# Kernel optimization log

Measured on AMD Instinct MI355X. Metric: run time of the kernel, lower is better.

Reference implementation:

```python
import jax, jax.numpy as jnp
import numpy as np

B, L, D = 8, 4096, 512  # batch, seq_len (power of 2), in_features
R_MIN, R_MAX = 0.9, 0.999


def setup_inputs() -> dict:
    key = jax.random.key(0)
    k1, k2, k3 = jax.random.split(key, 3)
    inputs = jax.random.normal(k1, (B, L, D), dtype=jnp.float32)
    # Linear layers: i_dense D->2D, o_dense 2D->D (torch Linear: y = x @ W.T + b)
    Wi = jax.random.normal(k2, (2 * D, D), dtype=jnp.float32) / np.sqrt(D)
    bi = jnp.zeros((2 * D,), dtype=jnp.float32)
    Wo = jax.random.normal(k3, (D, 2 * D), dtype=jnp.float32) / np.sqrt(2 * D)
    bo = jnp.zeros((D,), dtype=jnp.float32)
    # LRU param init, exactly as in the torch module
    rng = np.random.RandomState(0)
    u1 = rng.random_sample(D)
    u2 = rng.random_sample(D)
    v_log = np.log(-0.5 * np.log(u1 * (R_MAX ** 2 - R_MIN ** 2) + R_MIN ** 2))
    theta_log = np.log(u2 * np.pi * 2)
    gamma_log = np.log(np.sqrt(1 - np.exp(-np.exp(v_log)) ** 2))
    params_log = jnp.asarray(np.stack([v_log, theta_log, gamma_log]), dtype=jnp.float32)
    return {"inputs": inputs, "Wi": Wi, "bi": bi, "Wo": Wo, "bo": bo,
            "params_log": params_log}


def reference(inputs, Wi, bi, Wo, bo, params_log):
    b, lin, d = inputs.shape
    u = inputs @ Wi.T + bi                       # [B, L, 2D]
    params = jnp.exp(params_log)                 # [3, D]
    v, theta, gamma = params[0], params[1], params[2]
    log2_L = int(np.ceil(np.log2(lin)))
    Lp = 2 ** log2_L
    # interleaved (real, imag) pairs -> complex state
    u = u.reshape(b, lin, d, 2)
    x = jax.lax.complex(u[..., 0], u[..., 1])    # [B, L, D] complex64
    if Lp > lin:
        x = jnp.pad(x, ((0, 0), (0, Lp - lin), (0, 0)))
    # Blelloch-style doubling scan: after stage i, each block of length 2^i
    # holds the prefix-scanned values x_t = lam*x_{t-1} + u_t within the block.
    for i in range(1, log2_L + 1):
        l = 2 ** i
        xr = x.reshape(b * Lp // l, l, d)
        x1, x2 = xr[:, : l // 2], xr[:, l // 2 :]
        pos = jnp.arange(1, l // 2 + 1, dtype=jnp.float32)        # [l/2]
        lambs = jnp.exp(jax.lax.complex(-pos[:, None] * v,
                                        pos[:, None] * theta))   # [l/2, D]
        x2 = x2 + lambs * x1[:, -1:]
        x = jnp.concatenate([x1, x2], axis=1).reshape(b, Lp, d)
    x = x[:, :lin] * gamma.astype(jnp.complex64)
    xr = jnp.concatenate([jnp.real(x), jnp.imag(x)], axis=-1)     # [B, L, 2D]
    out = xr @ Wo.T + bo
    return jax.nn.relu(out)
```

## Files before the change

kernel.cpp:

```cpp
#include <hip/hip_runtime.h>
#include <cstdint>
#include <cstddef>

typedef unsigned short u16;
typedef unsigned int   u32;

typedef short bf16x8 __attribute__((ext_vector_type(8)));
typedef float f32x4  __attribute__((ext_vector_type(4)));

__device__ __forceinline__ u16 f2bf(float f) {
  u32 u = __float_as_uint(f);
  u += 0x7fffu + ((u >> 16) & 1u);
  return (u16)(u >> 16);
}
__device__ __forceinline__ float bflo(u32 w) { return __uint_as_float((w & 0xffffu) << 16); }
__device__ __forceinline__ float bfhi(u32 w) { return __uint_as_float(w & 0xffff0000u); }

#define GLB_AS(p) ((const __attribute__((address_space(1))) void*)(p))
#define LDS_AS(p) ((__attribute__((address_space(3))) void*)(p))

__global__ __launch_bounds__(256)
void conv3_f32_bf16(const float* __restrict__ in, u16* __restrict__ a,
                    const float* __restrict__ wi, u16* __restrict__ wib,
                    const float* __restrict__ wo, u16* __restrict__ wob)
{
  long i = (long)blockIdx.x * 256 + threadIdx.x;
  const float* src; u16* dst;
  if (i < 4194304L) { src = in; dst = a; }
  else if (i < 4325376L) { i -= 4194304L; src = wi; dst = wib; }
  else { i -= 4325376L; if (i >= 131072L) return; src = wo; dst = wob; }
  float4 v = ((const float4*)src)[i];
  u32 lo = (u32)f2bf(v.x) | ((u32)f2bf(v.y) << 16);
  u32 hi = (u32)f2bf(v.z) | ((u32)f2bf(v.w) << 16);
  ((uint2*)dst)[i] = make_uint2(lo, hi);
}

template<int N, int K, int LOGNB, int OUT_BF16, int RELU>
__global__ __launch_bounds__(512, 4)
void gemm_w2(const u16* __restrict__ A, const u16* __restrict__ Bw,
             const float* __restrict__ bias, void* __restrict__ Cout)
{
  __shared__ __align__(16) u16 As[3][256 * 32];
  __shared__ __align__(16) u16 Bs[3][128 * 32];

  const int tid  = threadIdx.x;
  const int lane = tid & 63;
  const int wave = tid >> 6;
  const int bid  = blockIdx.x;
  const int xcd  = bid & 7;
  const int s    = bid >> 3;
  const int m0 = (xcd * 16 + (s >> LOGNB)) * 256;
  const int n0 = (s & ((1 << LOGNB) - 1)) * 128;
  const int wm = (wave & 3) * 64;
  const int wn = (wave >> 2) * 64;

  f32x4 acc[4][4];
#pragma unroll
  for (int i = 0; i < 4; ++i)
#pragma unroll
    for (int j = 0; j < 4; ++j) acc[i][j] = f32x4{0.f, 0.f, 0.f, 0.f};

  const u16* Ap[2]; const u16* Bp; int ldsA[2]; int ldsB;
#pragma unroll
  for (int i = 0; i < 2; ++i) {
    int g = i * 512 + tid;
    int r = g >> 2;
    int koff = ((g & 3) ^ ((r >> 1) & 3)) << 3;
    Ap[i]   = A + (size_t)(m0 + r) * K + koff;
    ldsA[i] = (i * 512 + wave * 64) * 8;
  }
  {
    int g = tid;
    int r = g >> 2;
    int koff = ((g & 3) ^ ((r >> 1) & 3)) << 3;
    Bp   = Bw + (size_t)(n0 + r) * K + koff;
    ldsB = (wave * 64) * 8;
  }

  const int fm = lane & 15;
  const int q  = lane >> 4;
  int aoff[4], boff[4];
#pragma unroll
  for (int i = 0; i < 4; ++i) {
    int m = wm + i * 16 + fm;
    aoff[i] = (m * 4 + (q ^ ((m >> 1) & 3))) * 8;
    int n = wn + i * 16 + fm;
    boff[i] = (n * 4 + (q ^ ((n >> 1) & 3))) * 8;
  }

  auto stage = [&](int buf, int kt) {
    __builtin_amdgcn_global_load_lds(GLB_AS(Ap[0] + kt), LDS_AS(&As[buf][ldsA[0]]), 16, 0, 0);
    __builtin_amdgcn_global_load_lds(GLB_AS(Ap[1] + kt), LDS_AS(&As[buf][ldsA[1]]), 16, 0, 0);
    __builtin_amdgcn_global_load_lds(GLB_AS(Bp    + kt), LDS_AS(&Bs[buf][ldsB]),    16, 0, 0);
  };
  auto compute = [&](int buf) {
    bf16x8 af[4], bfr[4];
#pragma unroll
    for (int i = 0; i < 4; ++i) { af[i]  = *(const bf16x8*)&As[buf][aoff[i]];
                                  bfr[i] = *(const bf16x8*)&Bs[buf][boff[i]]; }
#pragma unroll
    for (int mi = 0; mi < 4; ++mi)
#pragma unroll
      for (int ni = 0; ni < 4; ++ni)
        acc[mi][ni] = __builtin_amdgcn_mfma_f32_16x16x32_bf16(af[mi], bfr[ni],
                                                              acc[mi][ni], 0, 0, 0);
  };

  constexpr int NT = K / 32;
  stage(0, 0);
  stage(1, 32);
#pragma unroll
  for (int t = 0; t < NT - 1; ++t) {
    asm volatile("s_waitcnt vmcnt(3)" ::: "memory");
    __builtin_amdgcn_s_barrier();
    if (t + 2 < NT) stage((t + 2) % 3, (t + 2) * 32);
    compute(t % 3);
  }
  asm volatile("s_waitcnt vmcnt(0)" ::: "memory");
  __builtin_amdgcn_s_barrier();
  compute((NT - 1) % 3);

  const int colL = lane & 15;
  const int rowQ = (lane >> 4) * 4;
#pragma unroll
  for (int mi = 0; mi < 4; ++mi) {
#pragma unroll
    for (int ni = 0; ni < 4; ++ni) {
      int col  = n0 + wn + ni * 16 + colL;
      int rowb = m0 + wm + mi * 16 + rowQ;
      float bv = bias[col];
#pragma unroll
      for (int r = 0; r < 4; ++r) {
        float v = acc[mi][ni][r] + bv;
        if (RELU) v = fmaxf(v, 0.f);
        size_t idx = (size_t)(rowb + r) * N + col;
        if (OUT_BF16) ((u16*)Cout)[idx] = f2bf(v);
        else          ((float*)Cout)[idx] = v;
      }
    }
  }
}

__global__ __launch_bounds__(256)
void scan_chunk_end(const u16* __restrict__ u, const float* __restrict__ plog,
                    float2* __restrict__ e)
{
  const int t = threadIdx.x;
  const int c = blockIdx.x;
  const int b = blockIdx.y;
  float2 vl = ((const float2*)plog)[t];
  float2 tl = ((const float2*)plog)[256 + t];
  float v0 = expf(vl.x), v1 = expf(vl.y);
  float t0 = expf(tl.x), t1 = expf(tl.y);
  float m0 = expf(-v0), m1 = expf(-v1);
  float lr0 = m0 * cosf(t0), li0 = m0 * sinf(t0);
  float lr1 = m1 * cosf(t1), li1 = m1 * sinf(t1);
  const uint2* up = (const uint2*)u;
  size_t idx = (size_t)(b * 4096 + c * 32) * 256 + t;
  float h0r = 0.f, h0i = 0.f, h1r = 0.f, h1i = 0.f;
#pragma unroll 8
  for (int s = 0; s < 32; ++s) {
    uint2 w = up[idx]; idx += 256;
    float u0r = bflo(w.x), u0i = bfhi(w.x);
    float u1r = bflo(w.y), u1i = bfhi(w.y);
    float n0r = fmaf(lr0, h0r, fmaf(-li0, h0i, u0r));
    float n0i = fmaf(lr0, h0i, fmaf( li0, h0r, u0i));
    float n1r = fmaf(lr1, h1r, fmaf(-li1, h1i, u1r));
    float n1i = fmaf(lr1, h1i, fmaf( li1, h1r, u1i));
    h0r = n0r; h0i = n0i; h1r = n1r; h1i = n1i;
  }
  ((float4*)e)[(size_t)(b * 128 + c) * 256 + t] = make_float4(h0r, h0i, h1r, h1i);
}

__global__ __launch_bounds__(256)
void scan_mid(const float* __restrict__ plog, float4* __restrict__ e)
{
  const int t = threadIdx.x;
  const int b = blockIdx.x;
  float2 vl = ((const float2*)plog)[t];
  float2 tl = ((const float2*)plog)[256 + t];
  float v0 = expf(vl.x), v1 = expf(vl.y);
  float t0 = expf(tl.x), t1 = expf(tl.y);
  float Lm0 = expf(-32.f * v0), Lm1 = expf(-32.f * v1);
  float La0 = 32.f * t0,        La1 = 32.f * t1;
  float Lr0 = Lm0 * cosf(La0), Li0 = Lm0 * sinf(La0);
  float Lr1 = Lm1 * cosf(La1), Li1 = Lm1 * sinf(La1);
  float h0r = 0.f, h0i = 0.f, h1r = 0.f, h1i = 0.f;
  size_t base = (size_t)(b * 128) * 256 + t;
#pragma unroll 4
  for (int c = 0; c < 128; ++c) {
    float4 ec = e[base + (size_t)c * 256];
    float n0r = fmaf(Lr0, h0r, fmaf(-Li0, h0i, ec.x));
    float n0i = fmaf(Lr0, h0i, fmaf( Li0, h0r, ec.y));
    float n1r = fmaf(Lr1, h1r, fmaf(-Li1, h1i, ec.z));
    float n1i = fmaf(Lr1, h1i, fmaf( Li1, h1r, ec.w));
    h0r = n0r; h0i = n0i; h1r = n1r; h1i = n1i;
    e[base + (size_t)c * 256] = make_float4(h0r, h0i, h1r, h1i);
  }
}

__global__ __launch_bounds__(256)
void scan_out2(const u16* __restrict__ u, const float* __restrict__ plog,
               const float4* __restrict__ e, u16* __restrict__ xr)
{
  const int t = threadIdx.x;
  const int c = blockIdx.x;
  const int b = blockIdx.y;
  float2 vl = ((const float2*)plog)[t];
  float2 tl = ((const float2*)plog)[256 + t];
  float2 gl = ((const float2*)plog)[512 + t];
  float v0 = expf(vl.x), v1 = expf(vl.y);
  float t0 = expf(tl.x), t1 = expf(tl.y);
  float g0 = expf(gl.x), g1 = expf(gl.y);
  float m0 = expf(-v0), m1 = expf(-v1);
  float lr0 = m0 * cosf(t0), li0 = m0 * sinf(t0);
  float lr1 = m1 * cosf(t1), li1 = m1 * sinf(t1);

  float h0r = 0.f, h0i = 0.f, h1r = 0.f, h1i = 0.f;
  if (c > 0) {
    float4 ec = e[(size_t)(b * 128 + c - 1) * 256 + t];
    h0r = ec.x; h0i = ec.y; h1r = ec.z; h1i = ec.w;
  }

  const uint2* up = (const uint2*)u;
  u32* xp = (u32*)xr;
  size_t uidx = (size_t)(b * 4096 + c * 32) * 256 + t;
  size_t xidx = (size_t)(b * 4096 + c * 32) * 512 + t;
#pragma unroll 8
  for (int s = 0; s < 32; ++s) {
    uint2 w = up[uidx]; uidx += 256;
    float u0r = bflo(w.x), u0i = bfhi(w.x);
    float u1r = bflo(w.y), u1i = bfhi(w.y);
    float n0r = fmaf(lr0, h0r, fmaf(-li0, h0i, u0r));
    float n0i = fmaf(lr0, h0i, fmaf( li0, h0r, u0i));
    float n1r = fmaf(lr1, h1r, fmaf(-li1, h1i, u1r));
    float n1i = fmaf(lr1, h1i, fmaf( li1, h1r, u1i));
    h0r = n0r; h0i = n0i; h1r = n1r; h1i = n1i;
    xp[xidx]       = (u32)f2bf(g0 * h0r) | ((u32)f2bf(g1 * h1r) << 16);
    xp[xidx + 256] = (u32)f2bf(g0 * h0i) | ((u32)f2bf(g1 * h1i) << 16);
    xidx += 512;
  }
}

extern "C" void kernel_launch(void* const* d_in, const int* in_sizes, int n_in,
                              void* d_out, int out_size, void* d_ws, size_t ws_size,
                              hipStream_t stream)
{
  (void)in_sizes; (void)n_in; (void)out_size; (void)ws_size;
  const float* inputs = (const float*)d_in[0];
  const float* Wi     = (const float*)d_in[1];
  const float* bi     = (const float*)d_in[2];
  const float* Wo     = (const float*)d_in[3];
  const float* bo     = (const float*)d_in[4];
  const float* plog   = (const float*)d_in[5];

  char* ws = (char*)d_ws;
  u16*    xrA   = (u16*)(ws);
  u16*    u_bf  = (u16*)(ws + 67108864ull);
  u16*    Wi_bf = (u16*)(ws + 134217728ull);
  u16*    Wo_bf = (u16*)(ws + 135266304ull);
  float2* e_b   = (float2*)(ws + 136314880ull);

  conv3_f32_bf16<<<17408, 256, 0, stream>>>(inputs, xrA, Wi, Wi_bf, Wo, Wo_bf);

  gemm_w2<1024, 512, 3, 1, 0><<<1024, 512, 0, stream>>>(xrA, Wi_bf, bi, u_bf);

  scan_chunk_end<<<dim3(128, 8), 256, 0, stream>>>(u_bf, plog, e_b);
  scan_mid<<<8, 256, 0, stream>>>(plog, (float4*)e_b);
  scan_out2<<<dim3(128, 8), 256, 0, stream>>>(u_bf, plog, (const float4*)e_b, xrA);

  gemm_w2<512, 1024, 2, 0, 1><<<512, 512, 0, stream>>>(xrA, Wo_bf, bo, d_out);
}
```

Before: 252.5 us.

## Fuse three-pass chunked scan into one kernel with flag-based decoupled lookback

Replaces the chunk-end, mid and output scan kernels with one kernel. Each block keeps its 32 timesteps of u in registers, publishes its local chunk-end state with a release flag, then spins on the flags of earlier chunks and combines their states using powers of lambda^32, processing four chunks at a time. This removes two launches, the serial scan_mid pass and the second read of u, at the cost of spin-waiting that relies on earlier blocks being scheduled first, a flags memset, and O(c) lookback work per block. The conversion kernel also becomes a grid-stride loop with fewer blocks.

After: 767.5 us. 204% more time.

```diff
diff --git a/kernel.cpp b/kernel.cpp
--- a/kernel.cpp
+++ b/kernel.cpp
@@ -24,15 +24,18 @@
                     const float* __restrict__ wi, u16* __restrict__ wib,
                     const float* __restrict__ wo, u16* __restrict__ wob)
 {
-  long i = (long)blockIdx.x * 256 + threadIdx.x;
-  const float* src; u16* dst;
-  if (i < 4194304L) { src = in; dst = a; }
-  else if (i < 4325376L) { i -= 4194304L; src = wi; dst = wib; }
-  else { i -= 4325376L; if (i >= 131072L) return; src = wo; dst = wob; }
-  float4 v = ((const float4*)src)[i];
-  u32 lo = (u32)f2bf(v.x) | ((u32)f2bf(v.y) << 16);
-  u32 hi = (u32)f2bf(v.z) | ((u32)f2bf(v.w) << 16);
-  ((uint2*)dst)[i] = make_uint2(lo, hi);
+  const long total = 4456448L;
+  for (long i = (long)blockIdx.x * 256 + threadIdx.x; i < total;
+       i += (long)gridDim.x * 256) {
+    long j = i; const float* src; u16* dst;
+    if (j < 4194304L) { src = in; dst = a; }
+    else if (j < 4325376L) { j -= 4194304L; src = wi; dst = wib; }
+    else { j -= 4325376L; src = wo; dst = wob; }
+    float4 v = ((const float4*)src)[j];
+    u32 lo = (u32)f2bf(v.x) | ((u32)f2bf(v.y) << 16);
+    u32 hi = (u32)f2bf(v.z) | ((u32)f2bf(v.w) << 16);
+    ((uint2*)dst)[j] = make_uint2(lo, hi);
+  }
 }
 
 template<int N, int K, int LOGNB, int OUT_BF16, int RELU>
@@ -142,70 +145,14 @@
 }
 
 __global__ __launch_bounds__(256)
-void scan_chunk_end(const u16* __restrict__ u, const float* __restrict__ plog,
-                    float2* __restrict__ e)
+void scan_fused(const u16* __restrict__ u, const float* __restrict__ plog,
+                float4* __restrict__ e, u32* __restrict__ flags,
+                u16* __restrict__ xr)
 {
   const int t = threadIdx.x;
   const int c = blockIdx.x;
   const int b = blockIdx.y;
-  float2 vl = ((const float2*)plog)[t];
-  float2 tl = ((const float2*)plog)[256 + t];
-  float v0 = expf(vl.x), v1 = expf(vl.y);
-  float t0 = expf(tl.x), t1 = expf(tl.y);
-  float m0 = expf(-v0), m1 = expf(-v1);
-  float lr0 = m0 * cosf(t0), li0 = m0 * sinf(t0);
-  float lr1 = m1 * cosf(t1), li1 = m1 * sinf(t1);
-  const uint2* up = (const uint2*)u;
-  size_t idx = (size_t)(b * 4096 + c * 32) * 256 + t;
-  float h0r = 0.f, h0i = 0.f, h1r = 0.f, h1i = 0.f;
-#pragma unroll 8
-  for (int s = 0; s < 32; ++s) {
-    uint2 w = up[idx]; idx += 256;
-    float u0r = bflo(w.x), u0i = bfhi(w.x);
-    float u1r = bflo(w.y), u1i = bfhi(w.y);
-    float n0r = fmaf(lr0, h0r, fmaf(-li0, h0i, u0r));
-    float n0i = fmaf(lr0, h0i, fmaf( li0, h0r, u0i));
-    float n1r = fmaf(lr1, h1r, fmaf(-li1, h1i, u1r));
-    float n1i = fmaf(lr1, h1i, fmaf( li1, h1r, u1i));
-    h0r = n0r; h0i = n0i; h1r = n1r; h1i = n1i;
-  }
-  ((float4*)e)[(size_t)(b * 128 + c) * 256 + t] = make_float4(h0r, h0i, h1r, h1i);
-}
-
-__global__ __launch_bounds__(256)
-void scan_mid(const float* __restrict__ plog, float4* __restrict__ e)
-{
-  const int t = threadIdx.x;
-  const int b = blockIdx.x;
-  float2 vl = ((const float2*)plog)[t];
-  float2 tl = ((const float2*)plog)[256 + t];
-  float v0 = expf(vl.x), v1 = expf(vl.y);
-  float t0 = expf(tl.x), t1 = expf(tl.y);
-  float Lm0 = expf(-32.f * v0), Lm1 = expf(-32.f * v1);
-  float La0 = 32.f * t0,        La1 = 32.f * t1;
-  float Lr0 = Lm0 * cosf(La0), Li0 = Lm0 * sinf(La0);
-  float Lr1 = Lm1 * cosf(La1), Li1 = Lm1 * sinf(La1);
-  float h0r = 0.f, h0i = 0.f, h1r = 0.f, h1i = 0.f;
-  size_t base = (size_t)(b * 128) * 256 + t;
-#pragma unroll 4
-  for (int c = 0; c < 128; ++c) {
-    float4 ec = e[base + (size_t)c * 256];
-    float n0r = fmaf(Lr0, h0r, fmaf(-Li0, h0i, ec.x));
-    float n0i = fmaf(Lr0, h0i, fmaf( Li0, h0r, ec.y));
-    float n1r = fmaf(Lr1, h1r, fmaf(-Li1, h1i, ec.z));
-    float n1i = fmaf(Lr1, h1i, fmaf( Li1, h1r, ec.w));
-    h0r = n0r; h0i = n0i; h1r = n1r; h1i = n1i;
-    e[base + (size_t)c * 256] = make_float4(h0r, h0i, h1r, h1i);
-  }
-}
-
-__global__ __launch_bounds__(256)
-void scan_out2(const u16* __restrict__ u, const float* __restrict__ plog,
-               const float4* __restrict__ e, u16* __restrict__ xr)
-{
-  const int t = threadIdx.x;
-  const int c = blockIdx.x;
-  const int b = blockIdx.y;
+
   float2 vl = ((const float2*)plog)[t];
   float2 tl = ((const float2*)plog)[256 + t];
   float2 gl = ((const float2*)plog)[512 + t];
@@ -216,21 +163,110 @@
   float lr0 = m0 * cosf(t0), li0 = m0 * sinf(t0);
   float lr1 = m1 * cosf(t1), li1 = m1 * sinf(t1);
 
+  const uint2* up = (const uint2*)u;
+  size_t uidx = (size_t)(b * 4096 + c * 32) * 256 + t;
+  uint2 ur[32];
+#pragma unroll
+  for (int s = 0; s < 32; ++s) { ur[s] = up[uidx]; uidx += 256; }
+
   float h0r = 0.f, h0i = 0.f, h1r = 0.f, h1i = 0.f;
+#pragma unroll
+  for (int s = 0; s < 32; ++s) {
+    float u0r = bflo(ur[s].x), u0i = bfhi(ur[s].x);
+    float u1r = bflo(ur[s].y), u1i = bfhi(ur[s].y);
+    float n0r = fmaf(lr0, h0r, fmaf(-li0, h0i, u0r));
+    float n0i = fmaf(lr0, h0i, fmaf( li0, h0r, u0i));
+    float n1r = fmaf(lr1, h1r, fmaf(-li1, h1i, u1r));
+    float n1i = fmaf(lr1, h1i, fmaf( li1, h1r, u1i));
+    h0r = n0r; h0i = n0i; h1r = n1r; h1i = n1i;
+  }
+
+  const int fbase = b * 128;
+  e[(size_t)(fbase + c) * 256 + t] = make_float4(h0r, h0i, h1r, h1i);
+  __syncthreads();
+  if (t == 0) {
+    __threadfence();
+    __hip_atomic_store(&flags[fbase + c], 1u, __ATOMIC_RELEASE,
+                       __HIP_MEMORY_SCOPE_AGENT);
+  }
+
+  float cr0 = 0.f, ci0 = 0.f, cr1 = 0.f, ci1 = 0.f;
   if (c > 0) {
-    float4 ec = e[(size_t)(b * 128 + c - 1) * 256 + t];
-    h0r = ec.x; h0i = ec.y; h1r = ec.z; h1i = ec.w;
-  }
-
-  const uint2* up = (const uint2*)u;
+    float Lm0 = expf(-32.f * v0), Lm1 = expf(-32.f * v1);
+    float La0 = 32.f * t0,        La1 = 32.f * t1;
+    float P1r0 = Lm0 * cosf(La0), P1i0 = Lm0 * sinf(La0);
+    float P1r1 = Lm1 * cosf(La1), P1i1 = Lm1 * sinf(La1);
+    float P2r0 = P1r0*P1r0 - P1i0*P1i0, P2i0 = 2.f*P1r0*P1i0;
+    float P2r1 = P1r1*P1r1 - P1i1*P1i1, P2i1 = 2.f*P1r1*P1i1;
+    float P3r0 = P2r0*P1r0 - P2i0*P1i0, P3i0 = P2r0*P1i0 + P2i0*P1r0;
+    float P3r1 = P2r1*P1r1 - P2i1*P1i1, P3i1 = P2r1*P1i1 + P2i1*P1r1;
+    float P4r0 = P2r0*P2r0 - P2i0*P2i0, P4i0 = 2.f*P2r0*P2i0;
+    float P4r1 = P2r1*P2r1 - P2i1*P2i1, P4i1 = 2.f*P2r1*P2i1;
+
+    float Wr0 = 1.f, Wi0 = 0.f, Wr1 = 1.f, Wi1 = 0.f;
+    int i = c - 1;
+    while (i >= 0 && (i & 3) != 3) {
+      if (t == 0)
+        while (__hip_atomic_load(&flags[fbase + i], __ATOMIC_ACQUIRE,
+                                 __HIP_MEMORY_SCOPE_AGENT) == 0u) {}
+      __syncthreads();
+      float4 ec = e[(size_t)(fbase + i) * 256 + t];
+      cr0 = fmaf(Wr0, ec.x, fmaf(-Wi0, ec.y, cr0));
+      ci0 = fmaf(Wr0, ec.y, fmaf( Wi0, ec.x, ci0));
+      cr1 = fmaf(Wr1, ec.z, fmaf(-Wi1, ec.w, cr1));
+      ci1 = fmaf(Wr1, ec.w, fmaf( Wi1, ec.z, ci1));
+      float nr0 = Wr0*P1r0 - Wi0*P1i0, ni0 = Wr0*P1i0 + Wi0*P1r0;
+      float nr1 = Wr1*P1r1 - Wi1*P1i1, ni1 = Wr1*P1i1 + Wi1*P1r1;
+      Wr0 = nr0; Wi0 = ni0; Wr1 = nr1; Wi1 = ni1;
+      --i;
+    }
+    while (i >= 3) {
+      int j = i - 3;
+      if (t == 0) {
+        for (;;) {
+          u32 f0 = __hip_atomic_load(&flags[fbase + j],     __ATOMIC_ACQUIRE, __HIP_MEMORY_SCOPE_AGENT);
+          u32 f1 = __hip_atomic_load(&flags[fbase + j + 1], __ATOMIC_ACQUIRE, __HIP_MEMORY_SCOPE_AGENT);
+          u32 f2 = __hip_atomic_load(&flags[fbase + j + 2], __ATOMIC_ACQUIRE, __HIP_MEMORY_SCOPE_AGENT);
+          u32 f3 = __hip_atomic_load(&flags[fbase + j + 3], __ATOMIC_ACQUIRE, __HIP_MEMORY_SCOPE_AGENT);
+          if (f0 & f1 & f2 & f3) break;
+        }
+      }
+      __syncthreads();
+      float4 e3 = e[(size_t)(fbase + i)     * 256 + t];
+      float4 e2 = e[(size_t)(fbase + i - 1) * 256 + t];
+      float4 e1 = e[(size_t)(fbase + i - 2) * 256 + t];
+      float4 e0 = e[(size_t)(fbase + i - 3) * 256 + t];
+      float a0r = e3.x, a0i = e3.y, a1r = e3.z, a1i = e3.w;
+      a0r = fmaf(P1r0, e2.x, fmaf(-P1i0, e2.y, a0r));
+      a0i = fmaf(P1r0, e2.y, fmaf( P1i0, e2.x, a0i));
+      a1r = fmaf(P1r1, e2.z, fmaf(-P1i1, e2.w, a1r));
+      a1i = fmaf(P1r1, e2.w, fmaf( P1i1, e2.z, a1i));
+      a0r = fmaf(P2r0, e1.x, fmaf(-P2i0, e1.y, a0r));
+      a0i = fmaf(P2r0, e1.y, fmaf( P2i0, e1.x, a0i));
+      a1r = fmaf(P2r1, e1.z, fmaf(-P2i1, e1.w, a1r));
+      a1i = fmaf(P2r1, e1.w, fmaf( P2i1, e1.z, a1i));
+      a0r = fmaf(P3r0, e0.x, fmaf(-P3i0, e0.y, a0r));
+      a0i = fmaf(P3r0, e0.y, fmaf( P3i0, e0.x, a0i));
+      a1r = fmaf(P3r1, e0.z, fmaf(-P3i1, e0.w, a1r));
+      a1i = fmaf(P3r1, e0.w, fmaf( P3i1, e0.z, a1i));
+      cr0 = fmaf(Wr0, a0r, fmaf(-Wi0, a0i, cr0));
+      ci0 = fmaf(Wr0, a0i, fmaf( Wi0, a0r, ci0));
+      cr1 = fmaf(Wr1, a1r, fmaf(-Wi1, a1i, cr1));
+      ci1 = fmaf(Wr1, a1i, fmaf( Wi1, a1r, ci1));
+      float nr0 = Wr0*P4r0 - Wi0*P4i0, ni0 = Wr0*P4i0 + Wi0*P4r0;
+      float nr1 = Wr1*P4r1 - Wi1*P4i1, ni1 = Wr1*P4i1 + Wi1*P4r1;
+      Wr0 = nr0; Wi0 = ni0; Wr1 = nr1; Wi1 = ni1;
+      i -= 4;
+    }
+  }
+
+  h0r = cr0; h0i = ci0; h1r = cr1; h1i = ci1;
   u32* xp = (u32*)xr;
-  size_t uidx = (size_t)(b * 4096 + c * 32) * 256 + t;
   size_t xidx = (size_t)(b * 4096 + c * 32) * 512 + t;
-#pragma unroll 8
+#pragma unroll
   for (int s = 0; s < 32; ++s) {
-    uint2 w = up[uidx]; uidx += 256;
-    float u0r = bflo(w.x), u0i = bfhi(w.x);
-    float u1r = bflo(w.y), u1i = bfhi(w.y);
+    float u0r = bflo(ur[s].x), u0i = bfhi(ur[s].x);
+    float u1r = bflo(ur[s].y), u1i = bfhi(ur[s].y);
     float n0r = fmaf(lr0, h0r, fmaf(-li0, h0i, u0r));
     float n0i = fmaf(lr0, h0i, fmaf( li0, h0r, u0i));
     float n1r = fmaf(lr1, h1r, fmaf(-li1, h1i, u1r));
@@ -259,15 +295,16 @@
   u16*    u_bf  = (u16*)(ws + 67108864ull);
   u16*    Wi_bf = (u16*)(ws + 134217728ull);
   u16*    Wo_bf = (u16*)(ws + 135266304ull);
-  float2* e_b   = (float2*)(ws + 136314880ull);
-
-  conv3_f32_bf16<<<17408, 256, 0, stream>>>(inputs, xrA, Wi, Wi_bf, Wo, Wo_bf);
+  float4* e_b   = (float4*)(ws + 136314880ull);
+  u32*    flags = (u32*)(ws + 140509184ull);
+
+  hipMemsetAsync(flags, 0, 8 * 128 * sizeof(u32), stream);
+
+  conv3_f32_bf16<<<4096, 256, 0, stream>>>(inputs, xrA, Wi, Wi_bf, Wo, Wo_bf);
 
   gemm_w2<1024, 512, 3, 1, 0><<<1024, 512, 0, stream>>>(xrA, Wi_bf, bi, u_bf);
 
-  scan_chunk_end<<<dim3(128, 8), 256, 0, stream>>>(u_bf, plog, e_b);
-  scan_mid<<<8, 256, 0, stream>>>(plog, (float4*)e_b);
-  scan_out2<<<dim3(128, 8), 256, 0, stream>>>(u_bf, plog, (const float4*)e_b, xrA);
+  scan_fused<<<dim3(128, 8), 256, 0, stream>>>(u_bf, plog, e_b, flags, xrA);
 
   gemm_w2<512, 1024, 2, 0, 1><<<512, 512, 0, stream>>>(xrA, Wo_bf, bo, d_out);
 }
```

## Rework GEMM to 256x256 tiles with BK=64 ping-pong quadrant schedule

Applied to the files above, without the earlier changes.

Replaces the 256x128 triple-buffered GEMM with a 256x256 tile, K-step of 64 and double buffering. Each wave now computes 128x64, and work is split into four MFMA quadrants interleaved with staged loads, barriers and setprio. The aim is better operand reuse per LDS byte and overlap of global loads with MFMA work. The cost is more registers (launch bounds lowered to 2 blocks per CU) and half as many blocks, which risks lower occupancy and worse tail balance, especially for the second GEMM with only 256 blocks.

New measurement: 274.4 us. +8.7%, slower.

```diff
diff --git a/kernel.cpp b/kernel.cpp
--- a/kernel.cpp
+++ b/kernel.cpp
@@ -36,12 +36,12 @@
 }
 
 template<int N, int K, int LOGNB, int OUT_BF16, int RELU>
-__global__ __launch_bounds__(512, 4)
-void gemm_w2(const u16* __restrict__ A, const u16* __restrict__ Bw,
+__global__ __launch_bounds__(512, 2)
+void gemm_8p(const u16* __restrict__ A, const u16* __restrict__ Bw,
              const float* __restrict__ bias, void* __restrict__ Cout)
 {
-  __shared__ __align__(16) u16 As[3][256 * 32];
-  __shared__ __align__(16) u16 Bs[3][128 * 32];
+  __shared__ __align__(16) u16 As[2][16384];
+  __shared__ __align__(16) u16 Bs[2][16384];
 
   const int tid  = threadIdx.x;
   const int lane = tid & 63;
@@ -50,88 +50,125 @@
   const int xcd  = bid & 7;
   const int s    = bid >> 3;
   const int m0 = (xcd * 16 + (s >> LOGNB)) * 256;
-  const int n0 = (s & ((1 << LOGNB) - 1)) * 128;
-  const int wm = (wave & 3) * 64;
-  const int wn = (wave >> 2) * 64;
-
-  f32x4 acc[4][4];
-#pragma unroll
-  for (int i = 0; i < 4; ++i)
+  const int n0 = (s & ((1 << LOGNB) - 1)) * 256;
+  const int wmr = (wave >> 2) * 128;
+  const int wn  = (wave & 3) * 64;
+
+  f32x4 acc[8][4];
+#pragma unroll
+  for (int i = 0; i < 8; ++i)
 #pragma unroll
     for (int j = 0; j < 4; ++j) acc[i][j] = f32x4{0.f, 0.f, 0.f, 0.f};
 
-  const u16* Ap[2]; const u16* Bp; int ldsA[2]; int ldsB;
-#pragma unroll
-  for (int i = 0; i < 2; ++i) {
-    int g = i * 512 + tid;
-    int r = g >> 2;
-    int koff = ((g & 3) ^ ((r >> 1) & 3)) << 3;
-    Ap[i]   = A + (size_t)(m0 + r) * K + koff;
-    ldsA[i] = (i * 512 + wave * 64) * 8;
-  }
-  {
-    int g = tid;
-    int r = g >> 2;
-    int koff = ((g & 3) ^ ((r >> 1) & 3)) << 3;
-    Bp   = Bw + (size_t)(n0 + r) * K + koff;
-    ldsB = (wave * 64) * 8;
-  }
+  const int koff = (((tid & 3) ^ ((tid >> 3) & 3)) << 3);
+  const u16* ApH[2]; const u16* BpH[2];
+#pragma unroll
+  for (int h = 0; h < 2; ++h) {
+    int r = 128 * h + (tid >> 2);
+    ApH[h] = A  + (size_t)(m0 + r) * K + koff;
+    BpH[h] = Bw + (size_t)(n0 + r) * K + koff;
+  }
+  const int ldsWave = wave * 64;
 
   const int fm = lane & 15;
   const int q  = lane >> 4;
-  int aoff[4], boff[4];
+  int aoffs[4][2], boffs[4][2];
 #pragma unroll
   for (int i = 0; i < 4; ++i) {
-    int m = wm + i * 16 + fm;
-    aoff[i] = (m * 4 + (q ^ ((m >> 1) & 3))) * 8;
-    int n = wn + i * 16 + fm;
-    boff[i] = (n * 4 + (q ^ ((n >> 1) & 3))) * 8;
-  }
-
-  auto stage = [&](int buf, int kt) {
-    __builtin_amdgcn_global_load_lds(GLB_AS(Ap[0] + kt), LDS_AS(&As[buf][ldsA[0]]), 16, 0, 0);
-    __builtin_amdgcn_global_load_lds(GLB_AS(Ap[1] + kt), LDS_AS(&As[buf][ldsA[1]]), 16, 0, 0);
-    __builtin_amdgcn_global_load_lds(GLB_AS(Bp    + kt), LDS_AS(&Bs[buf][ldsB]),    16, 0, 0);
-  };
-  auto compute = [&](int buf) {
-    bf16x8 af[4], bfr[4];
-#pragma unroll
-    for (int i = 0; i < 4; ++i) { af[i]  = *(const bf16x8*)&As[buf][aoff[i]];
-                                  bfr[i] = *(const bf16x8*)&Bs[buf][boff[i]]; }
-#pragma unroll
-    for (int mi = 0; mi < 4; ++mi)
-#pragma unroll
-      for (int ni = 0; ni < 4; ++ni)
-        acc[mi][ni] = __builtin_amdgcn_mfma_f32_16x16x32_bf16(af[mi], bfr[ni],
-                                                              acc[mi][ni], 0, 0, 0);
-  };
-
-  constexpr int NT = K / 32;
-  stage(0, 0);
-  stage(1, 32);
-#pragma unroll
-  for (int t = 0; t < NT - 1; ++t) {
-    asm volatile("s_waitcnt vmcnt(3)" ::: "memory");
-    __builtin_amdgcn_s_barrier();
-    if (t + 2 < NT) stage((t + 2) % 3, (t + 2) * 32);
-    compute(t % 3);
-  }
-  asm volatile("s_waitcnt vmcnt(0)" ::: "memory");
-  __builtin_amdgcn_s_barrier();
-  compute((NT - 1) % 3);
+    int m = wmr + i * 16 + fm;
+    int n = wn  + i * 16 + fm;
+#pragma unroll
+    for (int kk = 0; kk < 2; ++kk) {
+      aoffs[i][kk] = (kk * 1024 + m * 4 + (q ^ ((m >> 1) & 3))) * 8;
+      boffs[i][kk] = (kk * 1024 + n * 4 + (q ^ ((n >> 1) & 3))) * 8;
+    }
+  }
+
+  bf16x8 aH[4][2];
+  bf16x8 bF[4][2];
+
+  auto stageA = [&](int buf, int kt, int h) {
+#pragma unroll
+    for (int kk = 0; kk < 2; ++kk)
+      __builtin_amdgcn_global_load_lds(GLB_AS(ApH[h] + kt + kk * 32),
+          LDS_AS(&As[buf][(kk * 1024 + 512 * h + ldsWave) * 8]), 16, 0, 0);
+  };
+  auto stageB = [&](int buf, int kt, int h) {
+#pragma unroll
+    for (int kk = 0; kk < 2; ++kk)
+      __builtin_amdgcn_global_load_lds(GLB_AS(BpH[h] + kt + kk * 32),
+          LDS_AS(&Bs[buf][(kk * 1024 + 512 * h + ldsWave) * 8]), 16, 0, 0);
+  };
+  auto readA = [&](int buf, int mh) {
+#pragma unroll
+    for (int mf = 0; mf < 4; ++mf)
+#pragma unroll
+      for (int kk = 0; kk < 2; ++kk)
+        aH[mf][kk] = *(const bf16x8*)&As[buf][aoffs[mf][kk] + mh * 2048];
+  };
+  auto readB = [&](int buf, int nh) {
+#pragma unroll
+    for (int nf = 0; nf < 2; ++nf)
+#pragma unroll
+      for (int kk = 0; kk < 2; ++kk)
+        bF[nh * 2 + nf][kk] = *(const bf16x8*)&Bs[buf][boffs[nh * 2 + nf][kk]];
+  };
+  auto mfmaQ = [&](int mh, int nh) {
+#pragma unroll
+    for (int mf = 0; mf < 4; ++mf)
+#pragma unroll
+      for (int nf = 0; nf < 2; ++nf)
+#pragma unroll
+        for (int kk = 0; kk < 2; ++kk)
+          acc[mh * 4 + mf][nh * 2 + nf] =
+            __builtin_amdgcn_mfma_f32_16x16x32_bf16(aH[mf][kk], bF[nh * 2 + nf][kk],
+                                                    acc[mh * 4 + mf][nh * 2 + nf], 0, 0, 0);
+  };
+
+  constexpr int NT = K / 64;
+  stageA(0, 0, 0); stageA(0, 0, 1); stageB(0, 0, 0); stageB(0, 0, 1);
+  int cur = 0;
+  for (int t = 0; t < NT; ++t) {
+    const int nxt = cur ^ 1;
+    const bool pre = (t + 1 < NT);
+    const int ktn = (t + 1) * 64;
+    if (pre) { stageA(nxt, ktn, 0); stageB(nxt, ktn, 0); }
+    if (pre) asm volatile("s_waitcnt vmcnt(4)" ::: "memory");
+    else     asm volatile("s_waitcnt vmcnt(0)" ::: "memory");
+    __builtin_amdgcn_s_barrier();
+    readA(cur, 0); readB(cur, 0);
+    asm volatile("s_waitcnt lgkmcnt(0)" ::: "memory");
+    __builtin_amdgcn_sched_barrier(0);
+    __builtin_amdgcn_s_setprio(1); mfmaQ(0, 0); __builtin_amdgcn_s_setprio(0);
+    __builtin_amdgcn_s_barrier();
+    if (pre) { stageA(nxt, ktn, 1); stageB(nxt, ktn, 1); }
+    readB(cur, 1);
+    asm volatile("s_waitcnt lgkmcnt(0)" ::: "memory");
+    __builtin_amdgcn_sched_barrier(0);
+    __builtin_amdgcn_s_setprio(1); mfmaQ(0, 1); __builtin_amdgcn_s_setprio(0);
+    __builtin_amdgcn_s_barrier();
+    readA(cur, 1);
+    asm volatile("s_waitcnt lgkmcnt(0)" ::: "memory");
+    __builtin_amdgcn_sched_barrier(0);
+    __builtin_amdgcn_s_setprio(1); mfmaQ(1, 0); __builtin_amdgcn_s_setprio(0);
+    __builtin_amdgcn_s_barrier();
+    __builtin_amdgcn_s_setprio(1); mfmaQ(1, 1); __builtin_amdgcn_s_setprio(0);
+    __builtin_amdgcn_s_barrier();
+    cur = nxt;
+  }
 
   const int colL = lane & 15;
   const int rowQ = (lane >> 4) * 4;
 #pragma unroll
-  for (int mi = 0; mi < 4; ++mi) {
-#pragma unroll
-    for (int ni = 0; ni < 4; ++ni) {
-      int col  = n0 + wn + ni * 16 + colL;
-      int rowb = m0 + wm + mi * 16 + rowQ;
+  for (int mf = 0; mf < 8; ++mf) {
+#pragma unroll
+    for (int nf = 0; nf < 4; ++nf) {
+      int col  = n0 + wn + nf * 16 + colL;
+      int rowb = m0 + wmr + mf * 16 + rowQ;
       float bv = bias[col];
 #pragma unroll
       for (int r = 0; r < 4; ++r) {
-        float v = acc[mi][ni][r] + bv;
+        float v = acc[mf][nf][r] + bv;
         if (RELU) v = fmaxf(v, 0.f);
         size_t idx = (size_t)(rowb + r) * N + col;
         if (OUT_BF16) ((u16*)Cout)[idx] = f2bf(v);
@@ -263,11 +300,11 @@
 
   conv3_f32_bf16<<<17408, 256, 0, stream>>>(inputs, xrA, Wi, Wi_bf, Wo, Wo_bf);
 
-  gemm_w2<1024, 512, 3, 1, 0><<<1024, 512, 0, stream>>>(xrA, Wi_bf, bi, u_bf);
+  gemm_8p<1024, 512, 2, 1, 0><<<512, 512, 0, stream>>>(xrA, Wi_bf, bi, u_bf);
 
   scan_chunk_end<<<dim3(128, 8), 256, 0, stream>>>(u_bf, plog, e_b);
   scan_mid<<<8, 256, 0, stream>>>(plog, (float4*)e_b);
   scan_out2<<<dim3(128, 8), 256, 0, stream>>>(u_bf, plog, (const float4*)e_b, xrA);
 
-  gemm_w2<512, 1024, 2, 0, 1><<<512, 512, 0, stream>>>(xrA, Wo_bf, bo, d_out);
-}
+  gemm_8p<512, 1024, 1, 0, 1><<<256, 512, 0, stream>>>(xrA, Wo_bf, bo, d_out);
+}
```

## Fuse fp32-to-bf16 input conversion into the first GEMM's A-tile loading

Applied to the files above, without the earlier changes.

Drops the separate pass that converted the 64 MB fp32 activation tensor to bf16. The first GEMM now loads fp32 A tiles through registers, converts them to bf16 and writes them to LDS, while B still uses direct global-to-LDS loads. This removes a full read-write pass over the activations. In exchange the GEMM reads twice as many A bytes, uses register staging with a two-buffer pipeline instead of three, and per-element epilogue stores.

New measurement: 276.8 us. 1.1x slower.

```diff
diff --git a/kernel.cpp b/kernel.cpp
--- a/kernel.cpp
+++ b/kernel.cpp
@@ -20,19 +20,141 @@
 #define LDS_AS(p) ((__attribute__((address_space(3))) void*)(p))
 
 __global__ __launch_bounds__(256)
-void conv3_f32_bf16(const float* __restrict__ in, u16* __restrict__ a,
-                    const float* __restrict__ wi, u16* __restrict__ wib,
+void conv2_f32_bf16(const float* __restrict__ wi, u16* __restrict__ wib,
                     const float* __restrict__ wo, u16* __restrict__ wob)
 {
   long i = (long)blockIdx.x * 256 + threadIdx.x;
   const float* src; u16* dst;
-  if (i < 4194304L) { src = in; dst = a; }
-  else if (i < 4325376L) { i -= 4194304L; src = wi; dst = wib; }
-  else { i -= 4325376L; if (i >= 131072L) return; src = wo; dst = wob; }
+  if (i < 131072L) { src = wi; dst = wib; }
+  else { i -= 131072L; src = wo; dst = wob; }
   float4 v = ((const float4*)src)[i];
   u32 lo = (u32)f2bf(v.x) | ((u32)f2bf(v.y) << 16);
   u32 hi = (u32)f2bf(v.z) | ((u32)f2bf(v.w) << 16);
   ((uint2*)dst)[i] = make_uint2(lo, hi);
+}
+
+template<int N, int K, int LOGNB>
+__global__ __launch_bounds__(512, 4)
+void gemm_w1f(const float* __restrict__ Af, const u16* __restrict__ Bw,
+              const float* __restrict__ bias, u16* __restrict__ Cout)
+{
+  __shared__ __align__(16) u16 As[2][256 * 32];
+  __shared__ __align__(16) u16 Bs[2][128 * 32];
+
+  const int tid  = threadIdx.x;
+  const int lane = tid & 63;
+  const int wave = tid >> 6;
+  const int bid  = blockIdx.x;
+  const int xcd  = bid & 7;
+  const int s    = bid >> 3;
+  const int m0 = (xcd * 16 + (s >> LOGNB)) * 256;
+  const int n0 = (s & ((1 << LOGNB) - 1)) * 128;
+  const int wm = (wave & 3) * 64;
+  const int wn = (wave >> 2) * 64;
+
+  f32x4 acc[4][4];
+#pragma unroll
+  for (int i = 0; i < 4; ++i)
+#pragma unroll
+    for (int j = 0; j < 4; ++j) acc[i][j] = f32x4{0.f, 0.f, 0.f, 0.f};
+
+  const float* Asrc[2]; int gIdx[2];
+#pragma unroll
+  for (int i = 0; i < 2; ++i) {
+    int g = i * 512 + tid;
+    int r = g >> 2;
+    int o = (g & 3) ^ ((r >> 1) & 3);
+    Asrc[i] = Af + (size_t)(m0 + r) * K + o * 8;
+    gIdx[i] = g;
+  }
+  const u16* Bp; int ldsB;
+  {
+    int g = tid;
+    int r = g >> 2;
+    int koff = ((g & 3) ^ ((r >> 1) & 3)) << 3;
+    Bp   = Bw + (size_t)(n0 + r) * K + koff;
+    ldsB = (wave * 64) * 8;
+  }
+
+  const int fm = lane & 15;
+  const int q  = lane >> 4;
+  int aoff[4], boff[4];
+#pragma unroll
+  for (int i = 0; i < 4; ++i) {
+    int m = wm + i * 16 + fm;
+    aoff[i] = (m * 4 + (q ^ ((m >> 1) & 3))) * 8;
+    int n = wn + i * 16 + fm;
+    boff[i] = (n * 4 + (q ^ ((n >> 1) & 3))) * 8;
+  }
+
+  float4 ar[2][2];
+  auto loadA = [&](int kt) {
+#pragma unroll
+    for (int i = 0; i < 2; ++i) {
+      ar[i][0] = *(const float4*)(Asrc[i] + kt);
+      ar[i][1] = *(const float4*)(Asrc[i] + kt + 4);
+    }
+  };
+  auto writeA = [&](int buf) {
+#pragma unroll
+    for (int i = 0; i < 2; ++i) {
+      uint4 w;
+      w.x = (u32)f2bf(ar[i][0].x) | ((u32)f2bf(ar[i][0].y) << 16);
+      w.y = (u32)f2bf(ar[i][0].z) | ((u32)f2bf(ar[i][0].w) << 16);
+      w.z = (u32)f2bf(ar[i][1].x) | ((u32)f2bf(ar[i][1].y) << 16);
+      w.w = (u32)f2bf(ar[i][1].z) | ((u32)f2bf(ar[i][1].w) << 16);
+      *(uint4*)&As[buf][gIdx[i] * 8] = w;
+    }
+  };
+  auto stageB = [&](int buf, int kt) {
+    __builtin_amdgcn_global_load_lds(GLB_AS(Bp + kt), LDS_AS(&Bs[buf][ldsB]), 16, 0, 0);
+  };
+  auto compute = [&](int buf) {
+    bf16x8 af[4], bfr[4];
+#pragma unroll
+    for (int i = 0; i < 4; ++i) { af[i]  = *(const bf16x8*)&As[buf][aoff[i]];
+                                  bfr[i] = *(const bf16x8*)&Bs[buf][boff[i]]; }
+#pragma unroll
+    for (int mi = 0; mi < 4; ++mi)
+#pragma unroll
+      for (int ni = 0; ni < 4; ++ni)
+        acc[mi][ni] = __builtin_amdgcn_mfma_f32_16x16x32_bf16(af[mi], bfr[ni],
+                                                              acc[mi][ni], 0, 0, 0);
+  };
+
+  constexpr int NT = K / 32;
+  loadA(0); stageB(0, 0);
+  __syncthreads();
+  writeA(0);
+  __syncthreads();
+  int buf = 0;
+  for (int t = 0; t < NT; ++t) {
+    const bool pre = (t + 1 < NT);
+    if (pre) { loadA((t + 1) * 32); stageB(buf ^ 1, (t + 1) * 32); }
+    compute(buf);
+    __syncthreads();
+    if (pre) writeA(buf ^ 1);
+    __syncthreads();
+    buf ^= 1;
+  }
+
+  const int colL = lane & 15;
+  const int rowQ = (lane >> 4) * 4;
+#pragma unroll
+  for (int mi = 0; mi < 4; ++mi) {
+#pragma unroll
+    for (int ni = 0; ni < 4; ++ni) {
+      int col  = n0 + wn + ni * 16 + colL;
+      int rowb = m0 + wm + mi * 16 + rowQ;
+      float bv = bias[col];
+#pragma unroll
+      for (int r = 0; r < 4; ++r) {
+        float v = acc[mi][ni][r] + bv;
+        size_t idx = (size_t)(rowb + r) * N + col;
+        Cout[idx] = f2bf(v);
+      }
+    }
+  }
 }
 
 template<int N, int K, int LOGNB, int OUT_BF16, int RELU>
@@ -261,9 +383,9 @@
   u16*    Wo_bf = (u16*)(ws + 135266304ull);
   float2* e_b   = (float2*)(ws + 136314880ull);
 
-  conv3_f32_bf16<<<17408, 256, 0, stream>>>(inputs, xrA, Wi, Wi_bf, Wo, Wo_bf);
-
-  gemm_w2<1024, 512, 3, 1, 0><<<1024, 512, 0, stream>>>(xrA, Wi_bf, bi, u_bf);
+  conv2_f32_bf16<<<1024, 256, 0, stream>>>(Wi, Wi_bf, Wo, Wo_bf);
+
+  gemm_w1f<1024, 512, 3><<<1024, 512, 0, stream>>>(inputs, Wi_bf, bi, u_bf);
 
   scan_chunk_end<<<dim3(128, 8), 256, 0, stream>>>(u_bf, plog, e_b);
   scan_mid<<<8, 256, 0, stream>>>(plog, (float4*)e_b);
```
